# Performance work log

Measured on AMD Instinct MI355X. Metric: run time of the kernel, lower is better.

## Reference

```python
import jax, jax.numpy as jnp
import numpy as np

EMBED_DIM = 1024
NUM_HEADS = 16
HEAD_DIM = EMBED_DIM // NUM_HEADS


def setup_inputs() -> dict:
    key = jax.random.key(0)
    k_x, k_wqkv, k_bqkv, k_wp, k_bp = jax.random.split(key, 5)
    B, N, C = 4, 2048, EMBED_DIM
    bound_qkv = 1.0 / np.sqrt(C)
    bound_p = 1.0 / np.sqrt(C)
    return {
        "x": jax.random.normal(k_x, (B, N, C), dtype=jnp.float32),
        # nn.Linear stores weight as [out, in]; we keep that layout and use x @ W.T
        "w_qkv": jax.random.uniform(k_wqkv, (3 * C, C), jnp.float32, -bound_qkv, bound_qkv),
        "b_qkv": jax.random.uniform(k_bqkv, (3 * C,), jnp.float32, -bound_qkv, bound_qkv),
        "w_proj": jax.random.uniform(k_wp, (C, C), jnp.float32, -bound_p, bound_p),
        "b_proj": jax.random.uniform(k_bp, (C,), jnp.float32, -bound_p, bound_p),
    }


def reference(x, w_qkv, b_qkv, w_proj, b_proj):
    B, N, C = x.shape
    H, D = NUM_HEADS, HEAD_DIM
    qkv = x @ w_qkv.T + b_qkv                      # [B, N, 3C]
    qkv = qkv.reshape(B, N, 3, H, D)
    q = qkv[:, :, 0].transpose(0, 2, 1, 3)          # [B, H, N, D]
    k = qkv[:, :, 1].transpose(0, 2, 1, 3)
    v = qkv[:, :, 2].transpose(0, 2, 1, 3)
    scale = jnp.asarray(D, x.dtype) ** -0.5
    attn = jnp.einsum('bhqd,bhkd->bhqk', q, k) * scale  # [B, H, N, N]
    attn = jax.nn.softmax(attn, axis=-1)
    out = jnp.einsum('bhqk,bhkd->bhqd', attn, v)        # [B, H, N, D]
    out = out.transpose(0, 2, 1, 3).reshape(B, N, C)
    return out @ w_proj.T + b_proj
```

## Files before the change

kernel.cpp:

```cpp
#include <hip/hip_runtime.h>

typedef unsigned short u16;
typedef __attribute__((ext_vector_type(8))) short short8;
typedef __attribute__((ext_vector_type(4))) short s16x4;
typedef __attribute__((ext_vector_type(8))) _Float16 half8;
typedef __attribute__((ext_vector_type(4))) float f32x4;
typedef __attribute__((ext_vector_type(16))) float f32x16;
typedef __attribute__((ext_vector_type(4))) unsigned int u32x4;

#define DEVI static __device__ __forceinline__

static constexpr int B_ = 4, N_ = 2048, C_ = 1024, H_ = 16, D_ = 64;
static constexpr int M_ = B_ * N_;
static constexpr int C3 = 3072;

DEVI u16 f2h(float f) {
  _Float16 h = (_Float16)f;
  return __builtin_bit_cast(u16, h);
}

DEVI unsigned pk2h(float lo, float hi) {
  return __builtin_bit_cast(unsigned, __builtin_amdgcn_cvt_pkrtz(lo, hi));
}

DEVI void gload_lds16(const void* g, void* lds) {
  __builtin_amdgcn_global_load_lds(
      (const __attribute__((address_space(1))) unsigned int*)g,
      (__attribute__((address_space(3))) unsigned int*)lds, 16, 0, 0);
}

__global__ __launch_bounds__(256) void f32_to_f16(const float* __restrict__ src,
                                                  u16* __restrict__ dst, int n8) {
  int idx = blockIdx.x * 256 + threadIdx.x;
  if (idx >= n8) return;
  const float* s = src + (size_t)idx * 8;
  f32x4 f0 = *(const f32x4*)s;
  f32x4 f1 = *(const f32x4*)(s + 4);
  short8 o;
#pragma unroll
  for (int j = 0; j < 8; ++j) o[j] = (short)f2h(j < 4 ? f0[j] : f1[j - 4]);
  *(short8*)(dst + (size_t)idx * 8) = o;
}

template <bool OUT_F16>
__global__ __launch_bounds__(256) void gemm_bt(const u16* __restrict__ A,
                                               const u16* __restrict__ Bm,
                                               const float* __restrict__ bias,
                                               void* __restrict__ outp, int Nout) {
  __shared__ u16 As[128 * 32];
  __shared__ u16 Bs[128 * 32];
  const int tid = threadIdx.x;
  const int w = tid >> 6, l = tid & 63;
  const int wr = w >> 1, wc = w & 1;
  const int l15 = l & 15, lg = l >> 4;
  const int nx = gridDim.x;
  int bid = blockIdx.y * nx + blockIdx.x;
  int cpx = (nx * gridDim.y) >> 3;
  int swz = (bid & 7) * cpx + (bid >> 3);
  int bx = swz % nx, by = swz / nx;
  const u16* Ab = A + (size_t)(bx * 128) * C_;
  const u16* Bb = Bm + (size_t)(by * 128) * C_;
  const int arow = tid >> 2, ac8 = (tid & 3) * 8;
  f32x4 acc[4][4];
#pragma unroll
  for (int m = 0; m < 4; ++m)
#pragma unroll
    for (int n = 0; n < 4; ++n) acc[m][n] = (f32x4){0.f, 0.f, 0.f, 0.f};

  for (int kt = 0; kt < C_; kt += 32) {
    __syncthreads();
#pragma unroll
    for (int i = 0; i < 2; ++i) {
      gload_lds16(Ab + (size_t)(i * 64 + arow) * C_ + kt + ac8,
                  (char*)As + (i * 64 + w * 16) * 64);
      gload_lds16(Bb + (size_t)(i * 64 + arow) * C_ + kt + ac8,
                  (char*)Bs + (i * 64 + w * 16) * 64);
    }
    __syncthreads();
    half8 af[4], bf[4];
#pragma unroll
    for (int m = 0; m < 4; ++m)
      af[m] = __builtin_bit_cast(half8, *(const short8*)((const char*)As +
                  (wr * 64 + m * 16 + l15) * 64 + lg * 16));
#pragma unroll
    for (int n = 0; n < 4; ++n)
      bf[n] = __builtin_bit_cast(half8, *(const short8*)((const char*)Bs +
                  (wc * 64 + n * 16 + l15) * 64 + lg * 16));
#pragma unroll
    for (int m = 0; m < 4; ++m)
#pragma unroll
      for (int n = 0; n < 4; ++n)
        acc[m][n] = __builtin_amdgcn_mfma_f32_16x16x32_f16(af[m], bf[n], acc[m][n], 0, 0, 0);
  }
#pragma unroll
  for (int m = 0; m < 4; ++m)
#pragma unroll
    for (int n = 0; n < 4; ++n) {
      int col = by * 128 + wc * 64 + n * 16 + l15;
      float bval = bias[col];
#pragma unroll
      for (int i = 0; i < 4; ++i) {
        int row = bx * 128 + wr * 64 + m * 16 + lg * 4 + i;
        float v = acc[m][n][i] + bval;
        if (OUT_F16)
          ((u16*)outp)[(size_t)row * Nout + col] = f2h(v);
        else
          ((float*)outp)[(size_t)row * Nout + col] = v;
      }
    }
}

__global__ __launch_bounds__(256) void kfrag_prep(const u16* __restrict__ qkv,
                                                  u16* __restrict__ kf) {
  int g = blockIdx.x * 256 + threadIdx.x;
  int l = g & 63;
  int df = (g >> 6) & 3;
  int kh = (g >> 8) & 1;
  int t = (g >> 9) & 31;
  int bh = g >> 14;
  int b = bh >> 4, h = bh & 15;
  const u16* src = qkv + (size_t)(b * N_ + t * 64 + kh * 32 + (l & 31)) * C3 +
                   C_ + h * D_ + (df * 2 + (l >> 5)) * 8;
  *(short8*)(kf + (size_t)g * 8) = *(const short8*)src;
}

__global__ __launch_bounds__(256) void vfrag_prep(const u16* __restrict__ qkv,
                                                  u16* __restrict__ vf) {
  __shared__ u16 tile[64][72];
  const int tid = threadIdx.x;
  const int bh = blockIdx.y, b = bh >> 4, h = bh & 15;
  const int t = blockIdx.x;
  const int r = tid >> 3, c8 = (tid & 7) * 8;
#pragma unroll
  for (int rr = 0; rr < 2; ++rr) {
    int row = rr * 32 + r;
    short8 v = *(const short8*)(qkv + (size_t)(b * N_ + t * 64 + row) * C3 +
                                2 * C_ + h * D_ + c8);
    *(short8*)&tile[row][c8] = v;
  }
  __syncthreads();
  const int l = tid & 63, wv = tid >> 6;
  const int l31 = l & 31, hi = l >> 5;
#pragma unroll
  for (int i = 0; i < 2; ++i) {
    int combo = wv * 2 + i;
    int vh = combo >> 2, kc = combo & 3;
    short8 o;
#pragma unroll
    for (int jj = 0; jj < 8; ++jj)
      o[jj] = (short)tile[kc * 16 + (jj & 3) + 8 * (jj >> 2) + 4 * hi][vh * 32 + l31];
    *(short8*)(vf + ((size_t)(bh * 32 + t) * 8 + combo) * 512 + l * 8) = o;
  }
}

__global__ __launch_bounds__(256, 2) void attn_fused(const u16* __restrict__ qkv,
                                                     const u16* __restrict__ kf,
                                                     const u16* __restrict__ vf,
                                                     u16* __restrict__ att) {
  const int tid = threadIdx.x;
  const int w = tid >> 6, l = tid & 63;
  const int l31 = l & 31, hi = l >> 5;
  int bid = blockIdx.y * gridDim.x + blockIdx.x;
  int swz = (bid & 7) * 64 + (bid >> 3);
  const int qt = swz & 7, bh = swz >> 3;
  const int b = bh >> 4, h = bh & 15;
  const int qb = qt * 256 + w * 64;

  const float sc2 = 0.125f * 1.4426950408889634f;
  half8 qfA[4], qfB[4];
  {
    const _Float16 sch = (_Float16)sc2;
    const u16* qrowA = qkv + (size_t)(b * N_ + qb + l31) * C3 + h * D_ + hi * 8;
    const u16* qrowB = qrowA + (size_t)32 * C3;
#pragma unroll
    for (int df = 0; df < 4; ++df) {
      half8 qa = __builtin_bit_cast(half8, *(const short8*)(qrowA + df * 16));
      half8 qc = __builtin_bit_cast(half8, *(const short8*)(qrowB + df * 16));
#pragma unroll
      for (int j = 0; j < 8; ++j) { qa[j] *= sch; qc[j] *= sch; }
      qfA[df] = qa;
      qfB[df] = qc;
    }
  }

  f32x16 aA0, aA1, aB0, aB1;
#pragma unroll
  for (int j = 0; j < 16; ++j) { aA0[j] = 0.f; aA1[j] = 0.f; aB0[j] = 0.f; aB1[j] = 0.f; }
  float lrowA = 0.f, lrowB = 0.f;

  const u16* kp = kf + (size_t)bh * 32 * 4096;
  const u16* vp = vf + (size_t)bh * 32 * 4096;
  const int loff = l * 8;

#define MKPF(SV, J0, OUT)                                                      \
  {                                                                            \
    u32x4 wq = {pk2h(SV[J0 + 0], SV[J0 + 1]), pk2h(SV[J0 + 2], SV[J0 + 3]),   \
                pk2h(SV[J0 + 4], SV[J0 + 5]), pk2h(SV[J0 + 6], SV[J0 + 7])};   \
    OUT = __builtin_bit_cast(half8, wq);                                       \
  }

  for (int t = 0; t < 32; ++t) {
    const u16* kt = kp + t * 4096;
    const u16* vt = vp + t * 4096;

    half8 kfr[2][4];
#pragma unroll
    for (int kh = 0; kh < 2; ++kh)
#pragma unroll
      for (int df = 0; df < 4; ++df)
        kfr[kh][df] = __builtin_bit_cast(half8,
            *(const short8*)(kt + ((kh * 4 + df) * 64) * 8 + loff));

    f32x16 sA0, sA1;
#pragma unroll
    for (int j = 0; j < 16; ++j) { sA0[j] = 0.f; sA1[j] = 0.f; }
    __builtin_amdgcn_s_setprio(1);
#pragma unroll
    for (int df = 0; df < 4; ++df) {
      sA0 = __builtin_amdgcn_mfma_f32_32x32x16_f16(kfr[0][df], qfA[df], sA0, 0, 0, 0);
      sA1 = __builtin_amdgcn_mfma_f32_32x32x16_f16(kfr[1][df], qfA[df], sA1, 0, 0, 0);
    }
    __builtin_amdgcn_s_setprio(0);
    float suA[4] = {0.f, 0.f, 0.f, 0.f};
#pragma unroll
    for (int j = 0; j < 16; ++j) {
      sA0[j] = __builtin_amdgcn_exp2f(sA0[j]);
      suA[j & 3] += sA0[j];
    }
#pragma unroll
    for (int j = 0; j < 16; ++j) {
      sA1[j] = __builtin_amdgcn_exp2f(sA1[j]);
      suA[j & 3] += sA1[j];
    }
    lrowA += (suA[0] + suA[1]) + (suA[2] + suA[3]);
    half8 pfA0, pfA1, pfA2, pfA3;
    MKPF(sA0, 0, pfA0)
    MKPF(sA0, 8, pfA1)
    MKPF(sA1, 0, pfA2)
    MKPF(sA1, 8, pfA3)

    f32x16 sB0, sB1;
#pragma unroll
    for (int j = 0; j < 16; ++j) { sB0[j] = 0.f; sB1[j] = 0.f; }
    __builtin_amdgcn_s_setprio(1);
#pragma unroll
    for (int df = 0; df < 4; ++df) {
      sB0 = __builtin_amdgcn_mfma_f32_32x32x16_f16(kfr[0][df], qfB[df], sB0, 0, 0, 0);
      sB1 = __builtin_amdgcn_mfma_f32_32x32x16_f16(kfr[1][df], qfB[df], sB1, 0, 0, 0);
    }
    __builtin_amdgcn_s_setprio(0);

    half8 vfr[2][4];
#pragma unroll
    for (int vh = 0; vh < 2; ++vh)
#pragma unroll
      for (int kc = 0; kc < 4; ++kc)
        vfr[vh][kc] = __builtin_bit_cast(half8,
            *(const short8*)(vt + ((vh * 4 + kc) * 64) * 8 + loff));

    float suB[4] = {0.f, 0.f, 0.f, 0.f};
#pragma unroll
    for (int j = 0; j < 16; ++j) {
      sB0[j] = __builtin_amdgcn_exp2f(sB0[j]);
      suB[j & 3] += sB0[j];
    }
#pragma unroll
    for (int j = 0; j < 16; ++j) {
      sB1[j] = __builtin_amdgcn_exp2f(sB1[j]);
      suB[j & 3] += sB1[j];
    }
    lrowB += (suB[0] + suB[1]) + (suB[2] + suB[3]);
    half8 pfB0, pfB1, pfB2, pfB3;
    MKPF(sB0, 0, pfB0)
    MKPF(sB0, 8, pfB1)
    MKPF(sB1, 0, pfB2)
    MKPF(sB1, 8, pfB3)

    __builtin_amdgcn_s_setprio(1);
    aA0 = __builtin_amdgcn_mfma_f32_32x32x16_f16(vfr[0][0], pfA0, aA0, 0, 0, 0);
    aA1 = __builtin_amdgcn_mfma_f32_32x32x16_f16(vfr[1][0], pfA0, aA1, 0, 0, 0);
    aB0 = __builtin_amdgcn_mfma_f32_32x32x16_f16(vfr[0][0], pfB0, aB0, 0, 0, 0);
    aB1 = __builtin_amdgcn_mfma_f32_32x32x16_f16(vfr[1][0], pfB0, aB1, 0, 0, 0);
    aA0 = __builtin_amdgcn_mfma_f32_32x32x16_f16(vfr[0][1], pfA1, aA0, 0, 0, 0);
    aA1 = __builtin_amdgcn_mfma_f32_32x32x16_f16(vfr[1][1], pfA1, aA1, 0, 0, 0);
    aB0 = __builtin_amdgcn_mfma_f32_32x32x16_f16(vfr[0][1], pfB1, aB0, 0, 0, 0);
    aB1 = __builtin_amdgcn_mfma_f32_32x32x16_f16(vfr[1][1], pfB1, aB1, 0, 0, 0);
    aA0 = __builtin_amdgcn_mfma_f32_32x32x16_f16(vfr[0][2], pfA2, aA0, 0, 0, 0);
    aA1 = __builtin_amdgcn_mfma_f32_32x32x16_f16(vfr[1][2], pfA2, aA1, 0, 0, 0);
    aB0 = __builtin_amdgcn_mfma_f32_32x32x16_f16(vfr[0][2], pfB2, aB0, 0, 0, 0);
    aB1 = __builtin_amdgcn_mfma_f32_32x32x16_f16(vfr[1][2], pfB2, aB1, 0, 0, 0);
    aA0 = __builtin_amdgcn_mfma_f32_32x32x16_f16(vfr[0][3], pfA3, aA0, 0, 0, 0);
    aA1 = __builtin_amdgcn_mfma_f32_32x32x16_f16(vfr[1][3], pfA3, aA1, 0, 0, 0);
    aB0 = __builtin_amdgcn_mfma_f32_32x32x16_f16(vfr[0][3], pfB3, aB0, 0, 0, 0);
    aB1 = __builtin_amdgcn_mfma_f32_32x32x16_f16(vfr[1][3], pfB3, aB1, 0, 0, 0);
    __builtin_amdgcn_s_setprio(0);
  }
#undef MKPF

  {
    lrowA += __shfl_xor(lrowA, 32);
    lrowB += __shfl_xor(lrowB, 32);
    float rinvA = 1.0f / lrowA;
    float rinvB = 1.0f / lrowB;
    u16* orowA = att + (size_t)(b * N_ + qb + l31) * C_ + h * D_;
    u16* orowB = orowA + (size_t)32 * C_;
#pragma unroll
    for (int dt = 0; dt < 2; ++dt) {
#pragma unroll
      for (int r2 = 0; r2 < 4; ++r2) {
        int d0 = dt * 32 + r2 * 8 + hi * 4;
        s16x4 hvA, hvB;
#pragma unroll
        for (int i = 0; i < 4; ++i) {
          float vA = (dt ? aA1[r2 * 4 + i] : aA0[r2 * 4 + i]) * rinvA;
          float vB = (dt ? aB1[r2 * 4 + i] : aB0[r2 * 4 + i]) * rinvB;
          hvA[i] = (short)f2h(vA);
          hvB[i] = (short)f2h(vB);
        }
        *(s16x4*)(orowA + d0) = hvA;
        *(s16x4*)(orowB + d0) = hvB;
      }
    }
  }
}

extern "C" void kernel_launch(void* const* d_in, const int* in_sizes, int n_in,
                              void* d_out, int out_size, void* d_ws, size_t ws_size,
                              hipStream_t stream) {
  const float* x = (const float*)d_in[0];
  const float* w_qkv = (const float*)d_in[1];
  const float* b_qkv = (const float*)d_in[2];
  const float* w_proj = (const float*)d_in[3];
  const float* b_proj = (const float*)d_in[4];

  char* ws = (char*)d_ws;
  u16* qkv  = (u16*)(ws + 0);
  u16* x16  = (u16*)(ws + 50331648);
  u16* wq16 = (u16*)(ws + 67108864);
  u16* wp16 = (u16*)(ws + 73400320);
  u16* kf   = (u16*)(ws + 75497472);
  u16* vf   = (u16*)(ws + 92274688);
  u16* att  = (u16*)(ws + 109051904);

  f32_to_f16<<<4096, 256, 0, stream>>>(x, x16, M_ * C_ / 8);
  f32_to_f16<<<1536, 256, 0, stream>>>(w_qkv, wq16, 3 * C_ * C_ / 8);
  f32_to_f16<<<512, 256, 0, stream>>>(w_proj, wp16, C_ * C_ / 8);

  gemm_bt<true><<<dim3(64, 24), 256, 0, stream>>>(x16, wq16, b_qkv, qkv, C3);

  kfrag_prep<<<4096, 256, 0, stream>>>(qkv, kf);
  vfrag_prep<<<dim3(32, 64), 256, 0, stream>>>(qkv, vf);

  attn_fused<<<dim3(8, 64), 256, 0, stream>>>(qkv, kf, vf, att);

  gemm_bt<false><<<dim3(64, 8), 256, 0, stream>>>(att, wp16, b_proj, d_out, C_);
}
```

Before: 204.3 us.

## Double-buffer GEMM LDS with swizzle and merge prep kernels into fewer launches

The three fp32-to-fp16 conversion launches become one kernel, and the K and V fragment prep kernels are merged into one launch. This cuts launch overhead and tail gaps between small kernels. The GEMM now double-buffers its LDS tiles, prefetching the next K slice while computing the current one, so each iteration needs one barrier instead of two. It also XOR-swizzles the LDS column chunk to reduce bank conflicts on fragment reads, at the cost of twice the LDS per block.

```diff
diff --git a/kernel.cpp b/kernel.cpp
--- a/kernel.cpp
+++ b/kernel.cpp
@@ -29,17 +29,30 @@
       (__attribute__((address_space(3))) unsigned int*)lds, 16, 0, 0);
 }
 
-__global__ __launch_bounds__(256) void f32_to_f16(const float* __restrict__ src,
-                                                  u16* __restrict__ dst, int n8) {
+__global__ __launch_bounds__(256) void f32_to_f16_all(const float* __restrict__ x,
+                                                      const float* __restrict__ wq,
+                                                      const float* __restrict__ wp,
+                                                      u16* __restrict__ x16,
+                                                      u16* __restrict__ wq16,
+                                                      u16* __restrict__ wp16) {
   int idx = blockIdx.x * 256 + threadIdx.x;
-  if (idx >= n8) return;
-  const float* s = src + (size_t)idx * 8;
-  f32x4 f0 = *(const f32x4*)s;
-  f32x4 f1 = *(const f32x4*)(s + 4);
+  const float* s;
+  u16* d;
+  int base;
+  if (idx < 1048576) {
+    s = x; d = x16; base = idx;
+  } else if (idx < 1048576 + 393216) {
+    s = wq; d = wq16; base = idx - 1048576;
+  } else {
+    s = wp; d = wp16; base = idx - 1441792;
+  }
+  const float* sp = s + (size_t)base * 8;
+  f32x4 f0 = *(const f32x4*)sp;
+  f32x4 f1 = *(const f32x4*)(sp + 4);
   short8 o;
 #pragma unroll
   for (int j = 0; j < 8; ++j) o[j] = (short)f2h(j < 4 ? f0[j] : f1[j - 4]);
-  *(short8*)(dst + (size_t)idx * 8) = o;
+  *(short8*)(d + (size_t)base * 8) = o;
 }
 
 template <bool OUT_F16>
@@ -47,8 +60,8 @@
                                                const u16* __restrict__ Bm,
                                                const float* __restrict__ bias,
                                                void* __restrict__ outp, int Nout) {
-  __shared__ u16 As[128 * 32];
-  __shared__ u16 Bs[128 * 32];
+  __shared__ u16 As[2][128 * 32];
+  __shared__ u16 Bs[2][128 * 32];
   const int tid = threadIdx.x;
   const int w = tid >> 6, l = tid & 63;
   const int wr = w >> 1, wc = w & 1;
@@ -60,38 +73,49 @@
   int bx = swz % nx, by = swz / nx;
   const u16* Ab = A + (size_t)(bx * 128) * C_;
   const u16* Bb = Bm + (size_t)(by * 128) * C_;
-  const int arow = tid >> 2, ac8 = (tid & 3) * 8;
+  const int arow = tid >> 2;
+  const int ac8 = (((tid & 3) ^ ((tid >> 3) & 3)) * 8);
+  const int lgs = lg ^ ((l15 >> 1) & 3);
   f32x4 acc[4][4];
 #pragma unroll
   for (int m = 0; m < 4; ++m)
 #pragma unroll
     for (int n = 0; n < 4; ++n) acc[m][n] = (f32x4){0.f, 0.f, 0.f, 0.f};
 
-  for (int kt = 0; kt < C_; kt += 32) {
-    __syncthreads();
+  auto STAGE = [&](int t, int bb) {
+    const int kt = t * 32;
 #pragma unroll
     for (int i = 0; i < 2; ++i) {
       gload_lds16(Ab + (size_t)(i * 64 + arow) * C_ + kt + ac8,
-                  (char*)As + (i * 64 + w * 16) * 64);
+                  (char*)As[bb] + (i * 64 + w * 16) * 64);
       gload_lds16(Bb + (size_t)(i * 64 + arow) * C_ + kt + ac8,
-                  (char*)Bs + (i * 64 + w * 16) * 64);
-    }
-    __syncthreads();
+                  (char*)Bs[bb] + (i * 64 + w * 16) * 64);
+    }
+  };
+
+  STAGE(0, 0);
+  __syncthreads();
+  for (int t = 0; t < 32; ++t) {
+    if (t + 1 < 32) STAGE(t + 1, (t + 1) & 1);
+    const char* Ap = (const char*)As[t & 1];
+    const char* Bp = (const char*)Bs[t & 1];
     half8 af[4], bf[4];
 #pragma unroll
     for (int m = 0; m < 4; ++m)
-      af[m] = __builtin_bit_cast(half8, *(const short8*)((const char*)As +
-                  (wr * 64 + m * 16 + l15) * 64 + lg * 16));
+      af[m] = __builtin_bit_cast(half8, *(const short8*)(Ap +
+                  (wr * 64 + m * 16 + l15) * 64 + lgs * 16));
 #pragma unroll
     for (int n = 0; n < 4; ++n)
-      bf[n] = __builtin_bit_cast(half8, *(const short8*)((const char*)Bs +
-                  (wc * 64 + n * 16 + l15) * 64 + lg * 16));
+      bf[n] = __builtin_bit_cast(half8, *(const short8*)(Bp +
+                  (wc * 64 + n * 16 + l15) * 64 + lgs * 16));
 #pragma unroll
     for (int m = 0; m < 4; ++m)
 #pragma unroll
       for (int n = 0; n < 4; ++n)
         acc[m][n] = __builtin_amdgcn_mfma_f32_16x16x32_f16(af[m], bf[n], acc[m][n], 0, 0, 0);
-  }
+    __syncthreads();
+  }
+
 #pragma unroll
   for (int m = 0; m < 4; ++m)
 #pragma unroll
@@ -110,26 +134,28 @@
     }
 }
 
-__global__ __launch_bounds__(256) void kfrag_prep(const u16* __restrict__ qkv,
-                                                  u16* __restrict__ kf) {
-  int g = blockIdx.x * 256 + threadIdx.x;
-  int l = g & 63;
-  int df = (g >> 6) & 3;
-  int kh = (g >> 8) & 1;
-  int t = (g >> 9) & 31;
-  int bh = g >> 14;
-  int b = bh >> 4, h = bh & 15;
-  const u16* src = qkv + (size_t)(b * N_ + t * 64 + kh * 32 + (l & 31)) * C3 +
-                   C_ + h * D_ + (df * 2 + (l >> 5)) * 8;
-  *(short8*)(kf + (size_t)g * 8) = *(const short8*)src;
-}
-
-__global__ __launch_bounds__(256) void vfrag_prep(const u16* __restrict__ qkv,
-                                                  u16* __restrict__ vf) {
+__global__ __launch_bounds__(256) void kv_prep(const u16* __restrict__ qkv,
+                                               u16* __restrict__ kf,
+                                               u16* __restrict__ vf) {
   __shared__ u16 tile[64][72];
+  const int bxk = blockIdx.x;
+  if (bxk < 4096) {
+    int g = bxk * 256 + threadIdx.x;
+    int l = g & 63;
+    int df = (g >> 6) & 3;
+    int kh = (g >> 8) & 1;
+    int t = (g >> 9) & 31;
+    int bh = g >> 14;
+    int b = bh >> 4, h = bh & 15;
+    const u16* src = qkv + (size_t)(b * N_ + t * 64 + kh * 32 + (l & 31)) * C3 +
+                     C_ + h * D_ + (df * 2 + (l >> 5)) * 8;
+    *(short8*)(kf + (size_t)g * 8) = *(const short8*)src;
+    return;
+  }
+  const int idx2 = bxk - 4096;
+  const int t = idx2 & 31, bh = idx2 >> 5;
+  const int b = bh >> 4, h = bh & 15;
   const int tid = threadIdx.x;
-  const int bh = blockIdx.y, b = bh >> 4, h = bh & 15;
-  const int t = blockIdx.x;
   const int r = tid >> 3, c8 = (tid & 7) * 8;
 #pragma unroll
   for (int rr = 0; rr < 2; ++rr) {
@@ -342,14 +368,11 @@
   u16* vf   = (u16*)(ws + 92274688);
   u16* att  = (u16*)(ws + 109051904);
 
-  f32_to_f16<<<4096, 256, 0, stream>>>(x, x16, M_ * C_ / 8);
-  f32_to_f16<<<1536, 256, 0, stream>>>(w_qkv, wq16, 3 * C_ * C_ / 8);
-  f32_to_f16<<<512, 256, 0, stream>>>(w_proj, wp16, C_ * C_ / 8);
+  f32_to_f16_all<<<6144, 256, 0, stream>>>(x, w_qkv, w_proj, x16, wq16, wp16);
 
   gemm_bt<true><<<dim3(64, 24), 256, 0, stream>>>(x16, wq16, b_qkv, qkv, C3);
 
-  kfrag_prep<<<4096, 256, 0, stream>>>(qkv, kf);
-  vfrag_prep<<<dim3(32, 64), 256, 0, stream>>>(qkv, vf);
+  kv_prep<<<6144, 256, 0, stream>>>(qkv, kf, vf);
 
   attn_fused<<<dim3(8, 64), 256, 0, stream>>>(qkv, kf, vf, att);
 
```

After: 212.0 us. +3.8%, slower.
